# Optimization experiments

Hardware: AMD Instinct MI355X
Metric: run time of the kernel (lower is better)

The kernel has to match this reference:

```python
import jax, jax.numpy as jnp
import numpy as np


def setup_inputs() -> dict:
    key = jax.random.key(0)
    k1, k2 = jax.random.split(key)
    B, S, H, E = 8, 4096, 16, 64
    s = int(S ** 0.5)  # 64
    v = jax.random.normal(k1, (B, S, H, E), dtype=jnp.float32)
    w = jax.random.normal(k2, (1, H, 2 * s - 1), dtype=jnp.float32)  # 'full' bias base
    o_ = jnp.ones((s,), dtype=jnp.float32)
    return {"v": v, "w": w, "o_": o_}


def reference(v, w, o_):
    # FFTBias2d forward, bias_base_type='full', has_specials=False.
    B, S, H, E = v.shape
    s = int(S ** 0.5)  # grid side; S == s*s

    # z = w[..., shape_-seq_len : shape_+seq_len-1] with seq_len==shape_ -> whole w (len 2s-1)
    z = w[..., s - s : s + s - 1]          # (1, H, 2s-1)
    z_fft = jnp.fft.rfft(z)                # (1, H, s)

    # [B,S,H,E] -> [B,E,H,S] -> [B,E,H,s,s] -> [B,E,s,H,s]
    v_ = jnp.transpose(v, (0, 3, 2, 1)).reshape(B, E, H, s, s)
    v_ = jnp.transpose(v_, (0, 1, 3, 2, 4))

    # row-sum path: sum over first grid axis -> [B,E,H,s]
    v_s = v_.sum(-3)
    v_m = jnp.pad(v_s, ((0, 0), (0, 0), (0, 0), (s - 1, 0)))  # len 2s-1
    v_m_fft = jnp.fft.rfft(v_m)

    # col-sum path: [B,E,s2,H,s1] summed over s2 -> [B,E,H,s]
    u_s = jnp.transpose(v_, (0, 1, 4, 3, 2)).sum(-3)
    u_m = jnp.pad(u_s, ((0, 0), (0, 0), (0, 0), (s - 1, 0)))
    u_m_fft = jnp.fft.rfft(u_m)

    zf = jnp.expand_dims(z_fft, axis=1)    # (1, 1, H, s) broadcasts vs (B, E, H, s)
    RxV_m = jnp.fft.irfft(v_m_fft * zf)[..., :s]  # (B, E, H, s)
    RxU_m = jnp.fft.irfft(u_m_fft * zf)[..., :s]

    # outer sum over the two grid axes -> (B, E, H, s, s) -> (B, S, H, E)
    pbv = RxV_m[..., None, :] + RxU_m[..., :, None]
    pbv = pbv.reshape(B, E, H, S)
    pbv = jnp.transpose(pbv, (0, 3, 2, 1))

    # normalizer path
    o_pad = jnp.pad(o_, (s - 1, 0))        # len 2s-1
    o_fft = jnp.fft.rfft(o_pad)            # (s,)
    z_pb = jnp.fft.irfft(o_fft * z_fft)[..., :s] * s  # (1, H, s)
    z_pb = z_pb[..., None, :] + z_pb[..., :, None]    # (1, H, s, s)
    z_pb = z_pb.reshape(-1, H, S)
    z_pb = jnp.transpose(z_pb, (0, 2, 1))  # (1, S, H)
    return pbv, z_pb
```

## Files before the change

### kernel.cpp

```cpp
#include <hip/hip_runtime.h>
#include <stdint.h>

#define OUT2_OFF 33554432ull

typedef float v4f __attribute__((ext_vector_type(4)));

__device__ __forceinline__ v4f shflx4(v4f s, int m) {
    v4f r;
    r.x = __shfl_xor(s.x, m);
    r.y = __shfl_xor(s.y, m);
    r.z = __shfl_xor(s.z, m);
    r.w = __shfl_xor(s.w, m);
    return r;
}

__device__ __forceinline__ v4f reduce8(v4f* A, int rs) {
#pragma unroll
    for (int k = 0; k < 4; ++k) {
        v4f s = (rs & 2) ? A[k] : A[k + 4];
        v4f r = shflx4(s, 2);
        A[k] = ((rs & 2) ? A[k + 4] : A[k]) + r;
    }
#pragma unroll
    for (int k = 0; k < 2; ++k) {
        v4f s = (rs & 4) ? A[k] : A[k + 2];
        v4f r = shflx4(s, 4);
        A[k] = ((rs & 4) ? A[k + 2] : A[k]) + r;
    }
    v4f s = (rs & 8) ? A[0] : A[1];
    v4f r = shflx4(s, 8);
    return ((rs & 8) ? A[1] : A[0]) + r;
}

__global__ __launch_bounds__(256) void fused1_kernel(
        const float* __restrict__ v,
        const float* __restrict__ wgt,
        float* __restrict__ us,
        float* __restrict__ vs_part,
        float* __restrict__ G) {
    const int bid = blockIdx.x;
    const int tid = threadIdx.x;

    if (bid < 512) {
        const int ig = bid & 3, bh = bid >> 2;
        const int b = bh >> 4, h = bh & 15;
        const int w = tid >> 6, lane = tid & 63;
        const int rs = lane & 15;
        const int q  = 4 * w + (lane >> 4);

        const v4f* v4 = (const v4f*)v;
        const size_t base4 = (size_t)b * 1048576 + (size_t)h * 16 + q;

        v4f vsacc[4];
#pragma unroll
        for (int a = 0; a < 4; ++a) vsacc[a] = (v4f)0.f;
        v4f A[8], cur[4], nxt[4], R0;

#pragma unroll
        for (int jh = 0; jh < 4; ++jh)
            cur[jh] = __builtin_nontemporal_load(
                v4 + base4 + (size_t)(ig * 1024 + jh * 16 + rs) * 256);

#pragma unroll
        for (int il = 0; il < 16; ++il) {
            const int i = ig * 16 + il;
            if (il < 15) {
#pragma unroll
                for (int jh = 0; jh < 4; ++jh)
                    nxt[jh] = __builtin_nontemporal_load(
                        v4 + base4 + (size_t)((i + 1) * 64 + jh * 16 + rs) * 256);
            }
            v4f p = (cur[0] + cur[1]) + (cur[2] + cur[3]);
#pragma unroll
            for (int jh = 0; jh < 4; ++jh) vsacc[jh] += cur[jh];
            A[il & 7] = p;
            if (il == 7) R0 = reduce8(A, rs);
#pragma unroll
            for (int jh = 0; jh < 4; ++jh) cur[jh] = nxt[jh];
        }
        v4f R1 = reduce8(A, rs);
        {
            v4f s = (rs & 1) ? R0 : R1;
            v4f r = shflx4(s, 1);
            v4f res = ((rs & 1) ? R1 : R0) + r;
            const int ir = ((rs & 1) << 3) | (((rs >> 1) & 1) << 2) |
                           (((rs >> 2) & 1) << 1) | ((rs >> 3) & 1);
            *(v4f*)(us + ((size_t)bh * 64 + ig * 16 + ir) * 64 + q * 4) = res;
        }
#pragma unroll
        for (int jh = 0; jh < 4; ++jh) {
            const int j = jh * 16 + rs;
            *(v4f*)(vs_part + (((size_t)ig * 128 + bh) * 64 + j) * 64 + q * 4) =
                vsacc[jh];
        }
    } else {
        const int pb = bid - 512;
        const int h = pb >> 4, tq = pb & 15;
        __shared__ float zl[127];
        __shared__ float c127t[127], s127t[127];
        __shared__ float c126t[126], s126t[126];
        __shared__ float ZA[64], ZB[64];
        const float w127 = 6.28318530717958647692f / 127.0f;
        const float w126 = 6.28318530717958647692f / 126.0f;
        if (tid < 127) {
            zl[tid] = wgt[h * 127 + tid];
            float sv, cv; __sincosf((float)tid * w127, &sv, &cv);
            c127t[tid] = cv; s127t[tid] = sv;
        } else if (tid >= 128 && tid < 254) {
            const int m = tid - 128;
            float sv, cv; __sincosf((float)m * w126, &sv, &cv);
            c126t[m] = cv; s126t[m] = sv;
        }
        __syncthreads();
        if (tid < 64) {
            const int k = tid;
            float a = 0.f, bq = 0.f;
            int r = 0;
            for (int m = 0; m < 127; ++m) {
                a  += zl[m] * c127t[r];
                bq -= zl[m] * s127t[r];
                r += k; if (r >= 127) r -= 127;
            }
            ZA[k] = a; ZB[k] = bq;
        }
        __syncthreads();
        const int t = tq * 4 + (tid >> 6);
        const int j = tid & 63;
        const int jj = 63 + j;
        float acc = ZA[0];
        int rb = t, ra = jj;
        for (int k = 1; k <= 62; ++k) {
            const float cA = c126t[rb], sA = s126t[rb];
            const float cB = c127t[ra], sB = s127t[ra];
            const float cAB = cA * cB + sA * sB;
            const float sAB = sA * cB - cA * sB;
            acc += 2.f * (ZA[k] * cAB - ZB[k] * sAB);
            rb += t;  if (rb >= 126) rb -= 126;
            ra += jj; if (ra >= 127) ra -= 127;
        }
        {
            const int rn = (63 * jj) % 127;
            const float term = ZA[63] * c127t[rn] + ZB[63] * s127t[rn];
            acc += (t & 1) ? -term : term;
        }
        G[((size_t)h * 64 + t) * 64 + j] = acc * (1.0f / 126.0f);
    }
}

__global__ __launch_bounds__(256) void convemit_kernel(
        const float* __restrict__ G,
        const float* __restrict__ us,
        const float* __restrict__ vs_part,
        const float* __restrict__ ovec,
        float* __restrict__ out) {
    const int bid = blockIdx.x;
    const int tid = threadIdx.x;

    __shared__ __align__(16) float GlT[64 * 68];
    __shared__ __align__(16) float usl[4096];
    __shared__ __align__(16) float vsl[4096];
    __shared__ __align__(16) float rxv_l[64 * 68];
    __shared__ __align__(16) float rxu_l[16 * 68];
    __shared__ __align__(16) float zpb[1024];
    __shared__ __align__(16) float ol[64];

    if (bid < 512) {
        const int bh = bid >> 2, tq = bid & 3;
        const int b = bh >> 4, h = bh & 15;

        const v4f* usg = (const v4f*)(us + (size_t)bh * 4096);
        const v4f* vp0 = (const v4f*)(vs_part + (size_t)bh * 4096);
        const v4f* vp1 = (const v4f*)(vs_part + (size_t)(128 + bh) * 4096);
        const v4f* vp2 = (const v4f*)(vs_part + (size_t)(256 + bh) * 4096);
        const v4f* vp3 = (const v4f*)(vs_part + (size_t)(384 + bh) * 4096);
        const v4f* Gg  = (const v4f*)(G + (size_t)h * 4096);

#pragma unroll
        for (int k = 0; k < 4; ++k) {
            const int vi = k * 256 + tid;
            const int fi = vi * 4;
            v4f uu = usg[vi];
            *(v4f*)&usl[fi] = uu;
            v4f a = (vp0[vi] + vp1[vi]) + (vp2[vi] + vp3[vi]);
            *(v4f*)&vsl[fi] = a;
            v4f g = Gg[vi];
            const int t = fi >> 6, j0 = fi & 63;
            GlT[(j0 + 0) * 68 + t] = g.x;
            GlT[(j0 + 1) * 68 + t] = g.y;
            GlT[(j0 + 2) * 68 + t] = g.z;
            GlT[(j0 + 3) * 68 + t] = g.w;
        }
        __syncthreads();

        {
            const int tb = tid >> 4;
            const int q  = tid & 15;
            const int i_row = tq * 16 + tb;
            const v4f* us4 = (const v4f*)usl;
            const v4f* vs4 = (const v4f*)vsl;

            v4f accV[4];
#pragma unroll
            for (int r = 0; r < 4; ++r) accV[r] = (v4f)0.f;
            v4f accU = (v4f)0.f;
#pragma unroll 8
            for (int j = 0; j < 64; ++j) {
                const v4f gv = *(const v4f*)&GlT[j * 68 + tb * 4];
                const float gu = GlT[j * 68 + i_row];
                const v4f vv = vs4[j * 16 + q];
                const v4f uu = us4[j * 16 + q];
                accV[0] += gv.x * vv;
                accV[1] += gv.y * vv;
                accV[2] += gv.z * vv;
                accV[3] += gv.w * vv;
                accU += gu * uu;
            }
#pragma unroll
            for (int r = 0; r < 4; ++r)
                *(v4f*)&rxv_l[(tb * 4 + r) * 68 + q * 4] = accV[r];
            *(v4f*)&rxu_l[tb * 68 + q * 4] = accU;
        }
        __syncthreads();

        const int w = tid >> 6, lane = tid & 63;
        const int jsub = lane >> 4, qq = lane & 15;
        v4f rv4[4];
#pragma unroll
        for (int jj = 0; jj < 4; ++jj)
            rv4[jj] = *(const v4f*)&rxv_l[(jj * 16 + w * 4 + jsub) * 68 + qq * 4];
        const size_t obase =
            (((size_t)b * 4096 + tq * 1024) * 16 + h) * 64 + qq * 4;
        for (int il = 0; il < 16; ++il) {
            const v4f ru = *(const v4f*)&rxu_l[il * 68 + qq * 4];
#pragma unroll
            for (int jj = 0; jj < 4; ++jj) {
                const int j = jj * 16 + w * 4 + jsub;
                __builtin_nontemporal_store(rv4[jj] + ru,
                    (v4f*)(out + obase + (size_t)(il * 64 + j) * 1024));
            }
        }
    } else {
        const int bz = bid - 512;
        if (tid < 64) ol[tid] = ovec[tid];
        __syncthreads();
#pragma unroll
        for (int r = 0; r < 4; ++r) {
            const int idx = tid + 256 * r;
            const int h = idx >> 6, n = idx & 63;
            const v4f* G4 = (const v4f*)(G + (size_t)h * 4096 + n * 64);
            v4f acc4 = (v4f)0.f;
#pragma unroll
            for (int jv = 0; jv < 16; ++jv)
                acc4 += (*(const v4f*)&ol[jv * 4]) * G4[jv];
            zpb[idx] = (acc4.x + acc4.y + acc4.z + acc4.w) * 64.f;
        }
        __syncthreads();
#pragma unroll
        for (int r = 0; r < 4; ++r) {
            const int k = tid + 256 * r;
            const int hh = k & 15, c = k >> 4;
            out[OUT2_OFF + ((size_t)(bz * 64 + c)) * 16 + hh] =
                zpb[hh * 64 + c] + zpb[hh * 64 + bz];
        }
    }
}

extern "C" void kernel_launch(void* const* d_in, const int* in_sizes, int n_in,
                              void* d_out, int out_size, void* d_ws, size_t ws_size,
                              hipStream_t stream) {
    const float* v    = (const float*)d_in[0];
    const float* wgt  = (const float*)d_in[1];
    const float* ovec = (const float*)d_in[2];

    float* G       = (float*)d_ws;
    float* us      = G + 65536;
    float* vs_part = us + 524288;
    float* out     = (float*)d_out;

    hipLaunchKernelGGL(fused1_kernel,   dim3(512 + 256), dim3(256), 0, stream,
                       v, wgt, us, vs_part, G);
    hipLaunchKernelGGL(convemit_kernel, dim3(512 + 64),  dim3(256), 0, stream,
                       G, us, vs_part, ovec, out);
}
```

Before: 248.0 us.

## Restructure row/col-sum kernel access order and alias convemit shared memory via union

The reduction kernel now assigns each 16-thread group one grid row (j), so consecutive loads walk j-rows with deeper 8-deep prefetch. Column partial sums are reduced through cross-lane shuffles plus a small shared-memory tile combined across waves, replacing the earlier 16-lane butterfly. The second kernel overlays its three shared-memory phases in a union, with an extra barrier, which cuts LDS footprint and should allow more resident blocks. The tradeoffs are an added barrier and more registers held for the prefetch buffer.

```diff
diff --git a/kernel.cpp b/kernel.cpp
--- a/kernel.cpp
+++ b/kernel.cpp
@@ -12,24 +12,6 @@
     r.z = __shfl_xor(s.z, m);
     r.w = __shfl_xor(s.w, m);
     return r;
-}
-
-__device__ __forceinline__ v4f reduce8(v4f* A, int rs) {
-#pragma unroll
-    for (int k = 0; k < 4; ++k) {
-        v4f s = (rs & 2) ? A[k] : A[k + 4];
-        v4f r = shflx4(s, 2);
-        A[k] = ((rs & 2) ? A[k + 4] : A[k]) + r;
-    }
-#pragma unroll
-    for (int k = 0; k < 2; ++k) {
-        v4f s = (rs & 4) ? A[k] : A[k + 2];
-        v4f r = shflx4(s, 4);
-        A[k] = ((rs & 4) ? A[k + 2] : A[k]) + r;
-    }
-    v4f s = (rs & 8) ? A[0] : A[1];
-    v4f r = shflx4(s, 8);
-    return ((rs & 8) ? A[1] : A[0]) + r;
 }
 
 __global__ __launch_bounds__(256) void fused1_kernel(
@@ -41,65 +23,77 @@
     const int bid = blockIdx.x;
     const int tid = threadIdx.x;
 
+    __shared__ __align__(16) v4f upart[4][16][16];
+    __shared__ float zl[127];
+    __shared__ float c127t[127], s127t[127];
+    __shared__ float c126t[126], s126t[126];
+    __shared__ float ZA[64], ZB[64];
+
     if (bid < 512) {
         const int ig = bid & 3, bh = bid >> 2;
         const int b = bh >> 4, h = bh & 15;
-        const int w = tid >> 6, lane = tid & 63;
-        const int rs = lane & 15;
-        const int q  = 4 * w + (lane >> 4);
+        const int g = tid >> 4;
+        const int q = tid & 15;
+        const int w = tid >> 6;
+        const int lane = tid & 63;
+        const int s1 = (lane >> 4) & 1, s2 = (lane >> 5) & 1;
 
         const v4f* v4 = (const v4f*)v;
-        const size_t base4 = (size_t)b * 1048576 + (size_t)h * 16 + q;
-
-        v4f vsacc[4];
+        const size_t baseq =
+            (size_t)b * 1048576 + (size_t)(ig * 1024 + g) * 256 + h * 16 + q;
+
+        v4f vsacc[4], uacc[8], buf[8];
 #pragma unroll
         for (int a = 0; a < 4; ++a) vsacc[a] = (v4f)0.f;
-        v4f A[8], cur[4], nxt[4], R0;
-
+#pragma unroll
+        for (int a = 0; a < 8; ++a) uacc[a] = (v4f)0.f;
+
+#pragma unroll
+        for (int k0 = 0; k0 < 8; ++k0)
+            buf[k0] = __builtin_nontemporal_load(v4 + baseq + (size_t)k0 * 4096);
+
+#pragma unroll
+        for (int k = 0; k < 64; ++k) {
+            v4f c = buf[k & 7];
+            if (k < 56)
+                buf[k & 7] = __builtin_nontemporal_load(
+                    v4 + baseq + (size_t)(k + 8) * 4096);
+            vsacc[k & 3] += c;
+            uacc[(k >> 2) & 7] += c;
+            if ((k & 31) == 31) {
+                const int h0 = k >> 5;
+                v4f t4[4];
+#pragma unroll
+                for (int m = 0; m < 4; ++m) {
+                    v4f keep = s1 ? uacc[m + 4] : uacc[m];
+                    v4f send = s1 ? uacc[m] : uacc[m + 4];
+                    t4[m] = keep + shflx4(send, 16);
+                }
+#pragma unroll
+                for (int m = 0; m < 2; ++m) {
+                    v4f keep = s2 ? t4[m + 2] : t4[m];
+                    v4f send = s2 ? t4[m] : t4[m + 2];
+                    v4f r = keep + shflx4(send, 32);
+                    upart[w][h0 * 8 + m + 2 * s2 + 4 * s1][q] = r;
+                }
+#pragma unroll
+                for (int m = 0; m < 8; ++m) uacc[m] = (v4f)0.f;
+            }
+        }
 #pragma unroll
         for (int jh = 0; jh < 4; ++jh)
-            cur[jh] = __builtin_nontemporal_load(
-                v4 + base4 + (size_t)(ig * 1024 + jh * 16 + rs) * 256);
-
-#pragma unroll
-        for (int il = 0; il < 16; ++il) {
-            const int i = ig * 16 + il;
-            if (il < 15) {
-#pragma unroll
-                for (int jh = 0; jh < 4; ++jh)
-                    nxt[jh] = __builtin_nontemporal_load(
-                        v4 + base4 + (size_t)((i + 1) * 64 + jh * 16 + rs) * 256);
-            }
-            v4f p = (cur[0] + cur[1]) + (cur[2] + cur[3]);
-#pragma unroll
-            for (int jh = 0; jh < 4; ++jh) vsacc[jh] += cur[jh];
-            A[il & 7] = p;
-            if (il == 7) R0 = reduce8(A, rs);
-#pragma unroll
-            for (int jh = 0; jh < 4; ++jh) cur[jh] = nxt[jh];
-        }
-        v4f R1 = reduce8(A, rs);
+            *(v4f*)(vs_part + (((size_t)ig * 128 + bh) * 64 + g + 16 * jh) * 64 +
+                    q * 4) = vsacc[jh];
+        __syncthreads();
         {
-            v4f s = (rs & 1) ? R0 : R1;
-            v4f r = shflx4(s, 1);
-            v4f res = ((rs & 1) ? R1 : R0) + r;
-            const int ir = ((rs & 1) << 3) | (((rs >> 1) & 1) << 2) |
-                           (((rs >> 2) & 1) << 1) | ((rs >> 3) & 1);
-            *(v4f*)(us + ((size_t)bh * 64 + ig * 16 + ir) * 64 + q * 4) = res;
-        }
-#pragma unroll
-        for (int jh = 0; jh < 4; ++jh) {
-            const int j = jh * 16 + rs;
-            *(v4f*)(vs_part + (((size_t)ig * 128 + bh) * 64 + j) * 64 + q * 4) =
-                vsacc[jh];
+            const int i = tid >> 4, q2 = tid & 15;
+            v4f ssum = (upart[0][i][q2] + upart[1][i][q2]) +
+                       (upart[2][i][q2] + upart[3][i][q2]);
+            *(v4f*)(us + ((size_t)bh * 64 + ig * 16 + i) * 64 + q2 * 4) = ssum;
         }
     } else {
         const int pb = bid - 512;
         const int h = pb >> 4, tq = pb & 15;
-        __shared__ float zl[127];
-        __shared__ float c127t[127], s127t[127];
-        __shared__ float c126t[126], s126t[126];
-        __shared__ float ZA[64], ZB[64];
         const float w127 = 6.28318530717958647692f / 127.0f;
         const float w126 = 6.28318530717958647692f / 126.0f;
         if (tid < 127) {
@@ -147,6 +141,12 @@
     }
 }
 
+union K2Smem {
+    struct { float GlT[64 * 68]; float usl[4096]; float vsl[4096]; } a;
+    struct { float rxv[64 * 68]; float rxu[16 * 68]; } p2;
+    struct { float zpb[1024]; float ol[64]; } t;
+};
+
 __global__ __launch_bounds__(256) void convemit_kernel(
         const float* __restrict__ G,
         const float* __restrict__ us,
@@ -156,13 +156,7 @@
     const int bid = blockIdx.x;
     const int tid = threadIdx.x;
 
-    __shared__ __align__(16) float GlT[64 * 68];
-    __shared__ __align__(16) float usl[4096];
-    __shared__ __align__(16) float vsl[4096];
-    __shared__ __align__(16) float rxv_l[64 * 68];
-    __shared__ __align__(16) float rxu_l[16 * 68];
-    __shared__ __align__(16) float zpb[1024];
-    __shared__ __align__(16) float ol[64];
+    __shared__ __align__(16) K2Smem sm;
 
     if (bid < 512) {
         const int bh = bid >> 2, tq = bid & 3;
@@ -180,33 +174,32 @@
             const int vi = k * 256 + tid;
             const int fi = vi * 4;
             v4f uu = usg[vi];
-            *(v4f*)&usl[fi] = uu;
+            *(v4f*)&sm.a.usl[fi] = uu;
             v4f a = (vp0[vi] + vp1[vi]) + (vp2[vi] + vp3[vi]);
-            *(v4f*)&vsl[fi] = a;
+            *(v4f*)&sm.a.vsl[fi] = a;
             v4f g = Gg[vi];
             const int t = fi >> 6, j0 = fi & 63;
-            GlT[(j0 + 0) * 68 + t] = g.x;
-            GlT[(j0 + 1) * 68 + t] = g.y;
-            GlT[(j0 + 2) * 68 + t] = g.z;
-            GlT[(j0 + 3) * 68 + t] = g.w;
-        }
-        __syncthreads();
-
+            sm.a.GlT[(j0 + 0) * 68 + t] = g.x;
+            sm.a.GlT[(j0 + 1) * 68 + t] = g.y;
+            sm.a.GlT[(j0 + 2) * 68 + t] = g.z;
+            sm.a.GlT[(j0 + 3) * 68 + t] = g.w;
+        }
+        __syncthreads();
+
+        const int tb = tid >> 4;
+        const int q  = tid & 15;
+        const int i_row = tq * 16 + tb;
+        v4f accV[4];
+#pragma unroll
+        for (int r = 0; r < 4; ++r) accV[r] = (v4f)0.f;
+        v4f accU = (v4f)0.f;
         {
-            const int tb = tid >> 4;
-            const int q  = tid & 15;
-            const int i_row = tq * 16 + tb;
-            const v4f* us4 = (const v4f*)usl;
-            const v4f* vs4 = (const v4f*)vsl;
-
-            v4f accV[4];
-#pragma unroll
-            for (int r = 0; r < 4; ++r) accV[r] = (v4f)0.f;
-            v4f accU = (v4f)0.f;
+            const v4f* us4 = (const v4f*)sm.a.usl;
+            const v4f* vs4 = (const v4f*)sm.a.vsl;
 #pragma unroll 8
             for (int j = 0; j < 64; ++j) {
-                const v4f gv = *(const v4f*)&GlT[j * 68 + tb * 4];
-                const float gu = GlT[j * 68 + i_row];
+                const v4f gv = *(const v4f*)&sm.a.GlT[j * 68 + tb * 4];
+                const float gu = sm.a.GlT[j * 68 + i_row];
                 const v4f vv = vs4[j * 16 + q];
                 const v4f uu = us4[j * 16 + q];
                 accV[0] += gv.x * vv;
@@ -215,11 +208,12 @@
                 accV[3] += gv.w * vv;
                 accU += gu * uu;
             }
-#pragma unroll
-            for (int r = 0; r < 4; ++r)
-                *(v4f*)&rxv_l[(tb * 4 + r) * 68 + q * 4] = accV[r];
-            *(v4f*)&rxu_l[tb * 68 + q * 4] = accU;
-        }
+        }
+        __syncthreads();
+#pragma unroll
+        for (int r = 0; r < 4; ++r)
+            *(v4f*)&sm.p2.rxv[(tb * 4 + r) * 68 + q * 4] = accV[r];
+        *(v4f*)&sm.p2.rxu[tb * 68 + q * 4] = accU;
         __syncthreads();
 
         const int w = tid >> 6, lane = tid & 63;
@@ -227,11 +221,11 @@
         v4f rv4[4];
 #pragma unroll
         for (int jj = 0; jj < 4; ++jj)
-            rv4[jj] = *(const v4f*)&rxv_l[(jj * 16 + w * 4 + jsub) * 68 + qq * 4];
+            rv4[jj] = *(const v4f*)&sm.p2.rxv[(jj * 16 + w * 4 + jsub) * 68 + qq * 4];
         const size_t obase =
             (((size_t)b * 4096 + tq * 1024) * 16 + h) * 64 + qq * 4;
         for (int il = 0; il < 16; ++il) {
-            const v4f ru = *(const v4f*)&rxu_l[il * 68 + qq * 4];
+            const v4f ru = *(const v4f*)&sm.p2.rxu[il * 68 + qq * 4];
 #pragma unroll
             for (int jj = 0; jj < 4; ++jj) {
                 const int j = jj * 16 + w * 4 + jsub;
@@ -241,7 +235,7 @@
         }
     } else {
         const int bz = bid - 512;
-        if (tid < 64) ol[tid] = ovec[tid];
+        if (tid < 64) sm.t.ol[tid] = ovec[tid];
         __syncthreads();
 #pragma unroll
         for (int r = 0; r < 4; ++r) {
@@ -251,8 +245,8 @@
             v4f acc4 = (v4f)0.f;
 #pragma unroll
             for (int jv = 0; jv < 16; ++jv)
-                acc4 += (*(const v4f*)&ol[jv * 4]) * G4[jv];
-            zpb[idx] = (acc4.x + acc4.y + acc4.z + acc4.w) * 64.f;
+                acc4 += (*(const v4f*)&sm.t.ol[jv * 4]) * G4[jv];
+            sm.t.zpb[idx] = (acc4.x + acc4.y + acc4.z + acc4.w) * 64.f;
         }
         __syncthreads();
 #pragma unroll
@@ -260,7 +254,7 @@
             const int k = tid + 256 * r;
             const int hh = k & 15, c = k >> 4;
             out[OUT2_OFF + ((size_t)(bz * 64 + c)) * 16 + hh] =
-                zpb[hh * 64 + c] + zpb[hh * 64 + bz];
+                sm.t.zpb[hh * 64 + c] + sm.t.zpb[hh * 64 + bz];
         }
     }
 }
```

Result: faster. 240.9 us (-2.9%).
